# Kernel tuning notes

Hardware: AMD Instinct MI355X
Metric: run time of the kernel (lower is better)

The kernel has to match this reference:

```python
import jax, jax.numpy as jnp
import numpy as np

B, D, C = 16384, 1024, 2048


def setup_inputs() -> dict:
    key = jax.random.key(0)
    k1, k2 = jax.random.split(key)
    x = jax.random.normal(k1, (B, D), dtype=jnp.float32)
    # xavier_uniform for centers of shape (C, D): bound = sqrt(6/(C+D))
    bound = float(np.sqrt(6.0 / (C + D)))
    centers = jax.random.uniform(k2, (C, D), dtype=jnp.float32, minval=-bound, maxval=bound)
    gamma = jnp.ones((1,), dtype=jnp.float32)
    return {"x": x, "centers": centers, "gamma": gamma}


def _rbf(x, centers, gamma):
    # then Euclidean norm (sqrt) and exp(-gamma * dist) as in the torch module.
    x2 = jnp.sum(x * x, axis=-1, keepdims=True)            # (B, 1)
    c2 = jnp.sum(centers * centers, axis=-1)               # (C,)
    sq = x2 - 2.0 * jnp.einsum('bd,cd->bc', x, centers) + c2[None, :]
    dist = jnp.sqrt(jnp.maximum(sq, 0.0))                  # (B, C)
    return jnp.exp(-gamma[0] * dist)


def reference(x, centers, gamma):
    return _rbf(x, centers, gamma)
```

## Files before the change

kernel.cpp:

```cpp
#include <hip/hip_runtime.h>
#include <stdint.h>


typedef __attribute__((ext_vector_type(4))) int i32x4;

#define BM 128
#define BN 128
#define BK 128
#define KD 1024
#define NT 8

__global__ __launch_bounds__(256) void prep_i8_fused(
    const float* __restrict__ x, const float* __restrict__ cent,
    unsigned char* __restrict__ xq, unsigned char* __restrict__ cq,
    float2* __restrict__ xinfo, float2* __restrict__ cinfo,
    int Brows, int K) {
  int gid = blockIdx.x;
  const float* in;
  unsigned char* qb;
  float2* info;
  int row;
  if (gid < Brows) {
    in = x; qb = xq; info = xinfo; row = gid;
  } else {
    in = cent; qb = cq; info = cinfo; row = gid - Brows;
  }
  int tid = threadIdx.x;
  float4 v = ((const float4*)(in + (size_t)row * K))[tid];
  float ss = v.x * v.x + v.y * v.y + v.z * v.z + v.w * v.w;
  float am = fmaxf(fmaxf(fabsf(v.x), fabsf(v.y)), fmaxf(fabsf(v.z), fabsf(v.w)));
  for (int off = 32; off > 0; off >>= 1) {
    ss += __shfl_down(ss, off, 64);
    am = fmaxf(am, __shfl_down(am, off, 64));
  }
  __shared__ float pss[4], pam[4], sbc;
  int lane = tid & 63, w = tid >> 6;
  if (lane == 0) { pss[w] = ss; pam[w] = am; }
  __syncthreads();
  if (tid == 0) {
    float tss = pss[0] + pss[1] + pss[2] + pss[3];
    float tam = fmaxf(fmaxf(pam[0], pam[1]), fmaxf(pam[2], pam[3]));
    float s = tam > 0.f ? 127.f / tam : 0.f;
    info[row] = make_float2(tss, tam * (1.f / 127.f));
    sbc = s;
  }
  __syncthreads();
  float s = sbc;
  int qx = __float2int_rn(v.x * s), qy = __float2int_rn(v.y * s);
  int qz = __float2int_rn(v.z * s), qw = __float2int_rn(v.w * s);
  unsigned u = (unsigned)(qx & 255) | ((unsigned)(qy & 255) << 8) |
               ((unsigned)(qz & 255) << 16) | ((unsigned)(qw & 255) << 24);
  ((unsigned*)qb)[(size_t)row * (K >> 2) + tid] = u;
}

#define GLDS(gptr, lptr)                                                      \
  __builtin_amdgcn_global_load_lds(                                           \
      (const __attribute__((address_space(1))) unsigned int*)(gptr),          \
      (__attribute__((address_space(3))) unsigned int*)(lptr), 16, 0, 0)

#define DSR(dst, addr, imm)                                                   \
  asm volatile("ds_read_b128 %0, %1 offset:%c2"                              \
               : "=v"(dst) : "v"(addr), "i"(imm))

#define BARRIER __builtin_amdgcn_s_barrier()
#define LGKM(n)                                                               \
  do {                                                                        \
    asm volatile("s_waitcnt lgkmcnt(" #n ")" ::: "memory");                   \
    __builtin_amdgcn_sched_barrier(0);                                        \
  } while (0)
#define VMW(n) asm volatile("s_waitcnt vmcnt(" #n ")" ::: "memory")

#define MFMAI8(a, b, c) __builtin_amdgcn_mfma_i32_16x16x64_i8((a), (b), (c), 0, 0, 0)

__global__ __launch_bounds__(256) void rbf_gemm_i8(
    const unsigned char* __restrict__ A, const unsigned char* __restrict__ Bm,
    const float2* __restrict__ xinfo, const float2* __restrict__ cinfo,
    const float* __restrict__ gamma, float* __restrict__ out,
    int M, int N) {
  __shared__ __align__(16) unsigned char lds[2 * 32768];

  int nbn = N / BN;
  int nwg = (M / BM) * nbn;
  int bid = blockIdx.x;
  int wg = bid;
  if ((nwg & 7) == 0) {
    int cpx = nwg >> 3;
    wg = (bid & 7) * cpx + (bid >> 3);
  }
  int bm = wg / nbn, bn = wg % nbn;

  int tid = threadIdx.x;
  int lane = tid & 63, wv = tid >> 6;
  int wm = wv >> 1;
  int wn = wv & 1;
  int l15 = lane & 15, l4 = lane >> 4;

  const size_t Kz = (size_t)KD;

  int lsw = (tid & 7) ^ ((tid >> 3) & 7);
  const unsigned char* AgT = A + (size_t)bm * BM * Kz + (size_t)(tid >> 3) * Kz + lsw * 16;
  const unsigned char* BgT = Bm + (size_t)bn * BN * Kz + (size_t)(tid >> 3) * Kz + lsw * 16;
  const size_t r32 = (size_t)32 * Kz;

#define STG8(TAU, BUFS)                                                       \
  do {                                                                        \
    GLDS(AgT + (size_t)(TAU) * 128, (BUFS) + tid * 16);                       \
    GLDS(AgT + r32 + (size_t)(TAU) * 128, (BUFS) + 4096 + tid * 16);          \
    GLDS(AgT + 2 * r32 + (size_t)(TAU) * 128, (BUFS) + 8192 + tid * 16);      \
    GLDS(AgT + 3 * r32 + (size_t)(TAU) * 128, (BUFS) + 12288 + tid * 16);     \
    GLDS(BgT + (size_t)(TAU) * 128, (BUFS) + 16384 + tid * 16);               \
    GLDS(BgT + r32 + (size_t)(TAU) * 128, (BUFS) + 20480 + tid * 16);         \
    GLDS(BgT + 2 * r32 + (size_t)(TAU) * 128, (BUFS) + 24576 + tid * 16);     \
    GLDS(BgT + 3 * r32 + (size_t)(TAU) * 128, (BUFS) + 28672 + tid * 16);     \
  } while (0)

  int psl = l4 ^ (l15 & 7);
  unsigned ldsBase =
      (unsigned)(size_t)(const __attribute__((address_space(3))) void*)&lds[0];
  unsigned aBase = ldsBase + (unsigned)(wm * 8192 + l15 * 128 + psl * 16);
  unsigned bBase = ldsBase + (unsigned)(16384 + wn * 8192 + l15 * 128 + psl * 16);

  i32x4 acc[4][4];
#pragma unroll
  for (int m = 0; m < 4; ++m)
#pragma unroll
    for (int n = 0; n < 4; ++n) acc[m][n] = (i32x4){0, 0, 0, 0};

  STG8(0, lds);
  VMW(0);
  BARRIER;

#pragma unroll
  for (int t = 0; t < NT; ++t) {
    unsigned bufOff = (unsigned)(t & 1) * 32768u;
    unsigned char* bufS = lds + ((t + 1) & 1) * 32768;

    unsigned aAd0 = aBase + bufOff;
    unsigned bAd0 = bBase + bufOff;
    unsigned aAd1 = aAd0 ^ 64u;
    unsigned bAd1 = bAd0 ^ 64u;

    if (t + 1 < NT) STG8(t + 1, bufS);

    i32x4 a0, a1, a2, a3, b0, b1, b2, b3;
    i32x4 a4, a5, a6, a7, b4, b5, b6, b7;
    DSR(a0, aAd0, 0);    DSR(a1, aAd0, 2048);
    DSR(a2, aAd0, 4096); DSR(a3, aAd0, 6144);
    DSR(b0, bAd0, 0);    DSR(b1, bAd0, 2048);
    DSR(b2, bAd0, 4096); DSR(b3, bAd0, 6144);
    DSR(a4, aAd1, 0);    DSR(a5, aAd1, 2048);
    DSR(a6, aAd1, 4096); DSR(a7, aAd1, 6144);
    DSR(b4, bAd1, 0);    DSR(b5, bAd1, 2048);
    DSR(b6, bAd1, 4096); DSR(b7, bAd1, 6144);

    LGKM(8);
    __builtin_amdgcn_s_setprio(1);
    acc[0][0] = MFMAI8(a0, b0, acc[0][0]);
    acc[0][1] = MFMAI8(a0, b1, acc[0][1]);
    acc[0][2] = MFMAI8(a0, b2, acc[0][2]);
    acc[0][3] = MFMAI8(a0, b3, acc[0][3]);
    acc[1][0] = MFMAI8(a1, b0, acc[1][0]);
    acc[1][1] = MFMAI8(a1, b1, acc[1][1]);
    acc[1][2] = MFMAI8(a1, b2, acc[1][2]);
    acc[1][3] = MFMAI8(a1, b3, acc[1][3]);
    acc[2][0] = MFMAI8(a2, b0, acc[2][0]);
    acc[2][1] = MFMAI8(a2, b1, acc[2][1]);
    acc[2][2] = MFMAI8(a2, b2, acc[2][2]);
    acc[2][3] = MFMAI8(a2, b3, acc[2][3]);
    acc[3][0] = MFMAI8(a3, b0, acc[3][0]);
    acc[3][1] = MFMAI8(a3, b1, acc[3][1]);
    acc[3][2] = MFMAI8(a3, b2, acc[3][2]);
    acc[3][3] = MFMAI8(a3, b3, acc[3][3]);
    LGKM(0);
    acc[0][0] = MFMAI8(a4, b4, acc[0][0]);
    acc[0][1] = MFMAI8(a4, b5, acc[0][1]);
    acc[0][2] = MFMAI8(a4, b6, acc[0][2]);
    acc[0][3] = MFMAI8(a4, b7, acc[0][3]);
    acc[1][0] = MFMAI8(a5, b4, acc[1][0]);
    acc[1][1] = MFMAI8(a5, b5, acc[1][1]);
    acc[1][2] = MFMAI8(a5, b6, acc[1][2]);
    acc[1][3] = MFMAI8(a5, b7, acc[1][3]);
    acc[2][0] = MFMAI8(a6, b4, acc[2][0]);
    acc[2][1] = MFMAI8(a6, b5, acc[2][1]);
    acc[2][2] = MFMAI8(a6, b6, acc[2][2]);
    acc[2][3] = MFMAI8(a6, b7, acc[2][3]);
    acc[3][0] = MFMAI8(a7, b4, acc[3][0]);
    acc[3][1] = MFMAI8(a7, b5, acc[3][1]);
    acc[3][2] = MFMAI8(a7, b6, acc[3][2]);
    acc[3][3] = MFMAI8(a7, b7, acc[3][3]);
    __builtin_amdgcn_s_setprio(0);

    if (t < NT - 1) {
      VMW(0);
      BARRIER;
    }
  }

  float g = gamma[0];
  int rb0 = bm * BM + wm * 64 + l4 * 4;
  int cb0 = bn * BN + wn * 64 + l15;
#pragma unroll
  for (int m = 0; m < 4; ++m) {
#pragma unroll
    for (int j = 0; j < 4; ++j) {
      int row = rb0 + m * 16 + j;
      float2 xi = xinfo[row];
      size_t ob = (size_t)row * N;
#pragma unroll
      for (int n = 0; n < 4; ++n) {
        int col = cb0 + n * 16;
        float2 ci = cinfo[col];
        float dot = (float)acc[m][n][j] * xi.y * ci.y;
        float sq = fmaxf(xi.x + ci.x - 2.f * dot, 0.f);
        out[ob + col] = __expf(-g * __builtin_sqrtf(sq));
      }
    }
  }
}

__global__ __launch_bounds__(256) void rbf_naive(
    const float* __restrict__ x, const float* __restrict__ cent,
    const float* __restrict__ gamma, float* __restrict__ out, int D, int N) {
  int row = blockIdx.x;
  int col = blockIdx.y * blockDim.x + threadIdx.x;
  extern __shared__ float xs[];
  for (int i = threadIdx.x; i < D; i += blockDim.x)
    xs[i] = x[(size_t)row * D + i];
  __syncthreads();
  if (col >= N) return;
  const float* cp = cent + (size_t)col * D;
  float s = 0.f;
  for (int d = 0; d < D; ++d) {
    float df = xs[d] - cp[d];
    s += df * df;
  }
  out[(size_t)row * N + col] = __expf(-gamma[0] * __builtin_sqrtf(fmaxf(s, 0.f)));
}

extern "C" void kernel_launch(void* const* d_in, const int* in_sizes, int n_in,
                              void* d_out, int out_size, void* d_ws, size_t ws_size,
                              hipStream_t stream) {
  const float* x = (const float*)d_in[0];
  const float* cent = (const float*)d_in[1];
  const float* gamma = (const float*)d_in[2];
  float* out = (float*)d_out;

  const int D = 1024;
  int Brows = in_sizes[0] / D;
  int C = in_sizes[1] / D;

  size_t qa = (size_t)Brows * D;
  size_t qc = (size_t)C * D;
  size_t need = qa + qc + (size_t)Brows * 8 + (size_t)C * 8;
  bool can = (ws_size >= need) && (D == 1024) && (Brows % BM == 0) &&
             (C % BN == 0);

  if (!can) {
    dim3 grid(Brows, (C + 255) / 256);
    hipLaunchKernelGGL(rbf_naive, grid, dim3(256), D * sizeof(float), stream,
                       x, cent, gamma, out, D, C);
    return;
  }

  unsigned char* xb = (unsigned char*)d_ws;
  unsigned char* cb = xb + qa;
  float2* xinfo = (float2*)(xb + qa + qc);
  float2* cinfo = xinfo + Brows;

  hipLaunchKernelGGL(prep_i8_fused, dim3(Brows + C), dim3(256), 0, stream,
                     x, cent, xb, cb, xinfo, cinfo, Brows, D);

  int nwg = (Brows / BM) * (C / BN);
  hipLaunchKernelGGL(rbf_gemm_i8, dim3(nwg), dim3(256), 0, stream,
                     xb, cb, xinfo, cinfo, gamma, out, Brows, C);
}
```

Before: 81.60 us.

## Process four N-tiles per workgroup and prefetch next tile during epilogue

```diff
diff --git a/kernel.cpp b/kernel.cpp
--- a/kernel.cpp
+++ b/kernel.cpp
@@ -9,6 +9,7 @@
 #define BK 128
 #define KD 1024
 #define NT 8
+#define OT 4
 
 __global__ __launch_bounds__(256) void prep_i8_fused(
     const float* __restrict__ x, const float* __restrict__ cent,
@@ -79,15 +80,15 @@
     int M, int N) {
   __shared__ __align__(16) unsigned char lds[2 * 32768];
 
-  int nbn = N / BN;
-  int nwg = (M / BM) * nbn;
+  int nwg = (M / BM) * (N / BN) / OT;
   int bid = blockIdx.x;
   int wg = bid;
   if ((nwg & 7) == 0) {
     int cpx = nwg >> 3;
     wg = (bid & 7) * cpx + (bid >> 3);
   }
-  int bm = wg / nbn, bn = wg % nbn;
+  int bm = wg >> 2;
+  int bnBase = (wg & 3) * OT;
 
   int tid = threadIdx.x;
   int lane = tid & 63, wv = tid >> 6;
@@ -96,22 +97,24 @@
   int l15 = lane & 15, l4 = lane >> 4;
 
   const size_t Kz = (size_t)KD;
+  const size_t BNK = (size_t)BN * Kz;
 
   int lsw = (tid & 7) ^ ((tid >> 3) & 7);
   const unsigned char* AgT = A + (size_t)bm * BM * Kz + (size_t)(tid >> 3) * Kz + lsw * 16;
-  const unsigned char* BgT = Bm + (size_t)bn * BN * Kz + (size_t)(tid >> 3) * Kz + lsw * 16;
+  const unsigned char* BgT0 =
+      Bm + (size_t)bnBase * BNK + (size_t)(tid >> 3) * Kz + lsw * 16;
   const size_t r32 = (size_t)32 * Kz;
 
-#define STG8(TAU, BUFS)                                                       \
+#define STG8(TAU, BUFS, BP)                                                   \
   do {                                                                        \
     GLDS(AgT + (size_t)(TAU) * 128, (BUFS) + tid * 16);                       \
     GLDS(AgT + r32 + (size_t)(TAU) * 128, (BUFS) + 4096 + tid * 16);          \
     GLDS(AgT + 2 * r32 + (size_t)(TAU) * 128, (BUFS) + 8192 + tid * 16);      \
     GLDS(AgT + 3 * r32 + (size_t)(TAU) * 128, (BUFS) + 12288 + tid * 16);     \
-    GLDS(BgT + (size_t)(TAU) * 128, (BUFS) + 16384 + tid * 16);               \
-    GLDS(BgT + r32 + (size_t)(TAU) * 128, (BUFS) + 20480 + tid * 16);         \
-    GLDS(BgT + 2 * r32 + (size_t)(TAU) * 128, (BUFS) + 24576 + tid * 16);     \
-    GLDS(BgT + 3 * r32 + (size_t)(TAU) * 128, (BUFS) + 28672 + tid * 16);     \
+    GLDS((BP) + (size_t)(TAU) * 128, (BUFS) + 16384 + tid * 16);              \
+    GLDS((BP) + r32 + (size_t)(TAU) * 128, (BUFS) + 20480 + tid * 16);        \
+    GLDS((BP) + 2 * r32 + (size_t)(TAU) * 128, (BUFS) + 24576 + tid * 16);    \
+    GLDS((BP) + 3 * r32 + (size_t)(TAU) * 128, (BUFS) + 28672 + tid * 16);    \
   } while (0)
 
   int psl = l4 ^ (l15 & 7);
@@ -126,94 +129,112 @@
 #pragma unroll
     for (int n = 0; n < 4; ++n) acc[m][n] = (i32x4){0, 0, 0, 0};
 
-  STG8(0, lds);
+  float g = gamma[0];
+  int rb0 = bm * BM + wm * 64 + l4 * 4;
+
+  STG8(0, lds, BgT0);
   VMW(0);
   BARRIER;
 
-#pragma unroll
-  for (int t = 0; t < NT; ++t) {
-    unsigned bufOff = (unsigned)(t & 1) * 32768u;
-    unsigned char* bufS = lds + ((t + 1) & 1) * 32768;
-
-    unsigned aAd0 = aBase + bufOff;
-    unsigned bAd0 = bBase + bufOff;
-    unsigned aAd1 = aAd0 ^ 64u;
-    unsigned bAd1 = bAd0 ^ 64u;
-
-    if (t + 1 < NT) STG8(t + 1, bufS);
-
-    i32x4 a0, a1, a2, a3, b0, b1, b2, b3;
-    i32x4 a4, a5, a6, a7, b4, b5, b6, b7;
-    DSR(a0, aAd0, 0);    DSR(a1, aAd0, 2048);
-    DSR(a2, aAd0, 4096); DSR(a3, aAd0, 6144);
-    DSR(b0, bAd0, 0);    DSR(b1, bAd0, 2048);
-    DSR(b2, bAd0, 4096); DSR(b3, bAd0, 6144);
-    DSR(a4, aAd1, 0);    DSR(a5, aAd1, 2048);
-    DSR(a6, aAd1, 4096); DSR(a7, aAd1, 6144);
-    DSR(b4, bAd1, 0);    DSR(b5, bAd1, 2048);
-    DSR(b6, bAd1, 4096); DSR(b7, bAd1, 6144);
-
-    LGKM(8);
-    __builtin_amdgcn_s_setprio(1);
-    acc[0][0] = MFMAI8(a0, b0, acc[0][0]);
-    acc[0][1] = MFMAI8(a0, b1, acc[0][1]);
-    acc[0][2] = MFMAI8(a0, b2, acc[0][2]);
-    acc[0][3] = MFMAI8(a0, b3, acc[0][3]);
-    acc[1][0] = MFMAI8(a1, b0, acc[1][0]);
-    acc[1][1] = MFMAI8(a1, b1, acc[1][1]);
-    acc[1][2] = MFMAI8(a1, b2, acc[1][2]);
-    acc[1][3] = MFMAI8(a1, b3, acc[1][3]);
-    acc[2][0] = MFMAI8(a2, b0, acc[2][0]);
-    acc[2][1] = MFMAI8(a2, b1, acc[2][1]);
-    acc[2][2] = MFMAI8(a2, b2, acc[2][2]);
-    acc[2][3] = MFMAI8(a2, b3, acc[2][3]);
-    acc[3][0] = MFMAI8(a3, b0, acc[3][0]);
-    acc[3][1] = MFMAI8(a3, b1, acc[3][1]);
-    acc[3][2] = MFMAI8(a3, b2, acc[3][2]);
-    acc[3][3] = MFMAI8(a3, b3, acc[3][3]);
-    LGKM(0);
-    acc[0][0] = MFMAI8(a4, b4, acc[0][0]);
-    acc[0][1] = MFMAI8(a4, b5, acc[0][1]);
-    acc[0][2] = MFMAI8(a4, b6, acc[0][2]);
-    acc[0][3] = MFMAI8(a4, b7, acc[0][3]);
-    acc[1][0] = MFMAI8(a5, b4, acc[1][0]);
-    acc[1][1] = MFMAI8(a5, b5, acc[1][1]);
-    acc[1][2] = MFMAI8(a5, b6, acc[1][2]);
-    acc[1][3] = MFMAI8(a5, b7, acc[1][3]);
-    acc[2][0] = MFMAI8(a6, b4, acc[2][0]);
-    acc[2][1] = MFMAI8(a6, b5, acc[2][1]);
-    acc[2][2] = MFMAI8(a6, b6, acc[2][2]);
-    acc[2][3] = MFMAI8(a6, b7, acc[2][3]);
-    acc[3][0] = MFMAI8(a7, b4, acc[3][0]);
-    acc[3][1] = MFMAI8(a7, b5, acc[3][1]);
-    acc[3][2] = MFMAI8(a7, b6, acc[3][2]);
-    acc[3][3] = MFMAI8(a7, b7, acc[3][3]);
-    __builtin_amdgcn_s_setprio(0);
-
-    if (t < NT - 1) {
+  for (int ot = 0; ot < OT; ++ot) {
+    const unsigned char* BgT = BgT0 + (size_t)ot * BNK;
+
+#pragma unroll
+    for (int t = 0; t < NT; ++t) {
+      unsigned bufOff = (unsigned)(t & 1) * 32768u;
+      unsigned char* bufS = lds + ((t + 1) & 1) * 32768;
+
+      unsigned aAd0 = aBase + bufOff;
+      unsigned bAd0 = bBase + bufOff;
+      unsigned aAd1 = aAd0 ^ 64u;
+      unsigned bAd1 = bAd0 ^ 64u;
+
+      if (t + 1 < NT) {
+        STG8(t + 1, bufS, BgT);
+      } else if (ot + 1 < OT) {
+        STG8(0, bufS, BgT + BNK);
+      }
+
+      i32x4 a0, a1, a2, a3, b0, b1, b2, b3;
+      i32x4 a4, a5, a6, a7, b4, b5, b6, b7;
+      DSR(a0, aAd0, 0);    DSR(a1, aAd0, 2048);
+      DSR(a2, aAd0, 4096); DSR(a3, aAd0, 6144);
+      DSR(b0, bAd0, 0);    DSR(b1, bAd0, 2048);
+      DSR(b2, bAd0, 4096); DSR(b3, bAd0, 6144);
+      DSR(a4, aAd1, 0);    DSR(a5, aAd1, 2048);
+      DSR(a6, aAd1, 4096); DSR(a7, aAd1, 6144);
+      DSR(b4, bAd1, 0);    DSR(b5, bAd1, 2048);
+      DSR(b6, bAd1, 4096); DSR(b7, bAd1, 6144);
+
+      LGKM(8);
+      __builtin_amdgcn_s_setprio(1);
+      acc[0][0] = MFMAI8(a0, b0, acc[0][0]);
+      acc[0][1] = MFMAI8(a0, b1, acc[0][1]);
+      acc[0][2] = MFMAI8(a0, b2, acc[0][2]);
+      acc[0][3] = MFMAI8(a0, b3, acc[0][3]);
+      acc[1][0] = MFMAI8(a1, b0, acc[1][0]);
+      acc[1][1] = MFMAI8(a1, b1, acc[1][1]);
+      acc[1][2] = MFMAI8(a1, b2, acc[1][2]);
+      acc[1][3] = MFMAI8(a1, b3, acc[1][3]);
+      acc[2][0] = MFMAI8(a2, b0, acc[2][0]);
+      acc[2][1] = MFMAI8(a2, b1, acc[2][1]);
+      acc[2][2] = MFMAI8(a2, b2, acc[2][2]);
+      acc[2][3] = MFMAI8(a2, b3, acc[2][3]);
+      acc[3][0] = MFMAI8(a3, b0, acc[3][0]);
+      acc[3][1] = MFMAI8(a3, b1, acc[3][1]);
+      acc[3][2] = MFMAI8(a3, b2, acc[3][2]);
+      acc[3][3] = MFMAI8(a3, b3, acc[3][3]);
+      LGKM(0);
+      acc[0][0] = MFMAI8(a4, b4, acc[0][0]);
+      acc[0][1] = MFMAI8(a4, b5, acc[0][1]);
+      acc[0][2] = MFMAI8(a4, b6, acc[0][2]);
+      acc[0][3] = MFMAI8(a4, b7, acc[0][3]);
+      acc[1][0] = MFMAI8(a5, b4, acc[1][0]);
+      acc[1][1] = MFMAI8(a5, b5, acc[1][1]);
+      acc[1][2] = MFMAI8(a5, b6, acc[1][2]);
+      acc[1][3] = MFMAI8(a5, b7, acc[1][3]);
+      acc[2][0] = MFMAI8(a6, b4, acc[2][0]);
+      acc[2][1] = MFMAI8(a6, b5, acc[2][1]);
+      acc[2][2] = MFMAI8(a6, b6, acc[2][2]);
+      acc[2][3] = MFMAI8(a6, b7, acc[2][3]);
+      acc[3][0] = MFMAI8(a7, b4, acc[3][0]);
+      acc[3][1] = MFMAI8(a7, b5, acc[3][1]);
+      acc[3][2] = MFMAI8(a7, b6, acc[3][2]);
+      acc[3][3] = MFMAI8(a7, b7, acc[3][3]);
+      __builtin_amdgcn_s_setprio(0);
+
+      if (t < NT - 1) {
+        VMW(0);
+        BARRIER;
+      }
+    }
+
+    int cb0 = (bnBase + ot) * BN + wn * 64 + l15;
+#pragma unroll
+    for (int m = 0; m < 4; ++m) {
+#pragma unroll
+      for (int j = 0; j < 4; ++j) {
+        int row = rb0 + m * 16 + j;
+        float2 xi = xinfo[row];
+        size_t ob = (size_t)row * N;
+#pragma unroll
+        for (int n = 0; n < 4; ++n) {
+          int col = cb0 + n * 16;
+          float2 ci = cinfo[col];
+          float dot = (float)acc[m][n][j] * xi.y * ci.y;
+          float sq = fmaxf(xi.x + ci.x - 2.f * dot, 0.f);
+          out[ob + col] = __expf(-g * __builtin_sqrtf(sq));
+        }
+      }
+    }
+
+    if (ot + 1 < OT) {
+#pragma unroll
+      for (int m = 0; m < 4; ++m)
+#pragma unroll
+        for (int n = 0; n < 4; ++n) acc[m][n] = (i32x4){0, 0, 0, 0};
       VMW(0);
       BARRIER;
-    }
-  }
-
-  float g = gamma[0];
-  int rb0 = bm * BM + wm * 64 + l4 * 4;
-  int cb0 = bn * BN + wn * 64 + l15;
-#pragma unroll
-  for (int m = 0; m < 4; ++m) {
-#pragma unroll
-    for (int j = 0; j < 4; ++j) {
-      int row = rb0 + m * 16 + j;
-      float2 xi = xinfo[row];
-      size_t ob = (size_t)row * N;
-#pragma unroll
-      for (int n = 0; n < 4; ++n) {
-        int col = cb0 + n * 16;
-        float2 ci = cinfo[col];
-        float dot = (float)acc[m][n][j] * xi.y * ci.y;
-        float sq = fmaxf(xi.x + ci.x - 2.f * dot, 0.f);
-        out[ob + col] = __expf(-g * __builtin_sqrtf(sq));
-      }
     }
   }
 }
@@ -253,7 +274,7 @@
   size_t qc = (size_t)C * D;
   size_t need = qa + qc + (size_t)Brows * 8 + (size_t)C * 8;
   bool can = (ws_size >= need) && (D == 1024) && (Brows % BM == 0) &&
-             (C % BN == 0);
+             (C % (BN * OT) == 0);
 
   if (!can) {
     dim3 grid(Brows, (C + 255) / 256);
@@ -270,7 +291,7 @@
   hipLaunchKernelGGL(prep_i8_fused, dim3(Brows + C), dim3(256), 0, stream,
                      x, cent, xb, cb, xinfo, cinfo, Brows, D);
 
-  int nwg = (Brows / BM) * (C / BN);
+  int nwg = (Brows / BM) * (C / BN) / OT;
   hipLaunchKernelGGL(rbf_gemm_i8, dim3(nwg), dim3(256), 0, stream,
                      xb, cb, xinfo, cinfo, gamma, out, Brows, C);
 }
```

New measurement: 105.2 us. 29.0% more time.
